# Kernel optimization log

Measured on AMD Instinct MI355X. Metric: run time of the kernel, lower is better.

## Reference

```python
import jax, jax.numpy as jnp
import numpy as np

N_Q_HEADS = 16
N_KV_HEADS = 4
HEAD_DIM = 128
SLIDING_WINDOW = 1024
ROPE_BASE = 1024


def _rope_tables(L, dim):
    # half-truncate RoPE: first dim//4 freqs geometric, next dim//4 zero
    freqs = (1.0 / ROPE_BASE) ** jnp.linspace(0.0, 1.0, num=dim // 4)
    freqs = jnp.concatenate([freqs, jnp.zeros(dim // 4, dtype=freqs.dtype)])
    theta = jnp.arange(L, dtype=jnp.float32)[:, None] * freqs[None, :]  # (L, dim/2)
    cos = jnp.cos(theta)[None, :, None, :]  # (1, L, 1, dim/2)
    sin = jnp.sin(theta)[None, :, None, :]
    return cos, sin


def _rotate(x, cos, sin):
    # x: (B, L, H, D)
    x1, x2 = jnp.split(x, 2, axis=-1)
    return jnp.concatenate([x1 * cos + x2 * sin, -x1 * sin + x2 * cos], axis=-1)


def setup_inputs() -> dict:
    key = jax.random.key(0)
    k1, k2, k3, k4 = jax.random.split(key, 4)
    B, L, D = 1, 2048, 2048
    qkv_dim = (N_Q_HEADS + 2 * N_KV_HEADS) * HEAD_DIM  # 3072
    return {
        "x": jax.random.normal(k1, (B, L, D), dtype=jnp.float32),
        "Wqkv": jax.random.normal(k2, (D, qkv_dim), dtype=jnp.float32) * (D ** -0.5),
        "Wo": jax.random.normal(k3, (N_Q_HEADS * HEAD_DIM, D), dtype=jnp.float32) * ((N_Q_HEADS * HEAD_DIM) ** -0.5),
        "s": jax.random.normal(k4, (1, N_Q_HEADS), dtype=jnp.float32) * 0.1,
    }


def reference(x, Wqkv, Wo, s):
    B, L, D = x.shape
    H, QM, hd = N_KV_HEADS, N_Q_HEADS // N_KV_HEADS, HEAD_DIM

    proj = x @ Wqkv  # (B, L, (Hq + 2*Hkv) * hd)
    q, k, v = jnp.split(proj, (N_Q_HEADS * hd, (N_Q_HEADS + N_KV_HEADS) * hd), axis=-1)

    cos, sin = _rope_tables(L, hd)
    q = _rotate(q.reshape(B, L, -1, hd), cos, sin).reshape(B, L, H, QM, hd)
    k = _rotate(k.reshape(B, L, H, hd), cos, sin)
    v = v.reshape(B, L, H, hd)

    sm_scale = 1.0 / jnp.sqrt(jnp.float32(hd))
    q_pos = jnp.arange(L)[None, :, None]
    k_pos = jnp.arange(L)[None, None, :]
    causal = q_pos >= k_pos                       # (1, L, L)
    window = q_pos < k_pos + SLIDING_WINDOW       # index % 2 == 0 -> window active
    mask = causal & window

    # (B, H, M, Lq, Lk) attention logits
    attn = jnp.einsum("bqhmd,bkhd->bhmqk", q, k) * sm_scale
    # NOTE: faithful to source: -inf placed WHERE mask is True
    attn = jnp.where(mask, -jnp.inf, attn)

    sink = jnp.broadcast_to(s.reshape(B, H, QM, 1, 1), (B, H, QM, L, 1))
    w = jax.nn.softmax(jnp.concatenate([attn, sink], axis=-1), axis=-1)[..., :-1]

    out = jnp.einsum("bhmqk,bkhd->bqhmd", w, v).reshape(B, L, -1)
    return out @ Wo
```

## Files before the change

kernel.cpp:

```cpp
#include <hip/hip_runtime.h>
#include <hip/hip_bf16.h>
#include <math.h>

typedef __bf16 bf16;
typedef __bf16 bf16x8 __attribute__((ext_vector_type(8)));
typedef __bf16 bf16x4v __attribute__((ext_vector_type(4)));
typedef short s16x4 __attribute__((ext_vector_type(4)));
typedef float f32x4 __attribute__((ext_vector_type(4)));

#define GLD16(gp, lp) __builtin_amdgcn_global_load_lds( \
    (__attribute__((address_space(1))) void*)(void*)(gp), \
    (__attribute__((address_space(3))) void*)(lp), 16, 0, 0)

#define L_SEQ 2048
#define D_MODEL 2048
#define QKV_N 3072
#define HD 128
#define QSCALE 0.1275310242959836f
#define LOG2E 1.4426950408889634f

__global__ __launch_bounds__(256) void prep(const float* __restrict__ x,
                                            const float* __restrict__ Wqkv,
                                            const float* __restrict__ Wo,
                                            bf16* __restrict__ xb,
                                            bf16* __restrict__ wqkvT,
                                            bf16* __restrict__ woT) {
    __shared__ float tile[32][33];
    int bid = blockIdx.x;
    if (bid < 4096) {
        int idx = (bid * 256 + threadIdx.x) * 4;
        float4 f = *(const float4*)(x + idx);
        bf16x4v o;
        o.x = (bf16)f.x; o.y = (bf16)f.y; o.z = (bf16)f.z; o.w = (bf16)f.w;
        *(bf16x4v*)(xb + idx) = o;
        return;
    }
    bid -= 4096;
    const float* src; bf16* dst; long ld_s, ld_d; int bx, by;
    if (bid < 6144) { bx = bid % 96; by = bid / 96; src = Wqkv; dst = wqkvT; ld_s = QKV_N; ld_d = D_MODEL; }
    else { bid -= 6144; bx = bid & 63; by = bid >> 6; src = Wo; dst = woT; ld_s = D_MODEL; ld_d = D_MODEL; }
    const int tx = threadIdx.x & 31, ty = threadIdx.x >> 5;
    const long c = bx * 32 + tx, r0 = by * 32;
#pragma unroll
    for (int i = 0; i < 4; ++i)
        tile[ty + i * 8][tx] = src[(r0 + ty + i * 8) * ld_s + c];
    __syncthreads();
    const long c0 = bx * 32;
#pragma unroll
    for (int i = 0; i < 4; ++i)
        dst[(c0 + ty + i * 8) * ld_d + r0 + tx] = (bf16)tile[tx][ty + i * 8];
}

__global__ __launch_bounds__(256, 3) void gemm_qkv(const bf16* __restrict__ A,
                                                   const bf16* __restrict__ Bt,
                                                   bf16* __restrict__ Qb,
                                                   bf16* __restrict__ Kb,
                                                   bf16* __restrict__ Vtb) {
    constexpr int KDIM = D_MODEL;
    __shared__ __align__(16) bf16 As[2][64 * 64];
    __shared__ __align__(16) bf16 Bs[2][128 * 64];
    const int tid = threadIdx.x;
    const int wid = tid >> 6, lane = tid & 63;
    const int quad = lane >> 4, l15 = lane & 15;
    const int wm = wid & 1, wn = wid >> 1;
    const int head = blockIdx.x;
    const long m0 = (long)blockIdx.y * 64, n0 = (long)head * 128;

    f32x4 acc[2][4];
#pragma unroll
    for (int i = 0; i < 2; ++i)
#pragma unroll
        for (int j = 0; j < 4; ++j) acc[i][j] = (f32x4){0.f, 0.f, 0.f, 0.f};

    const int srow8 = lane >> 3;
    const int schunk = lane & 7;

    auto stage = [&](int k0, int buf) {
#pragma unroll
        for (int ii = 0; ii < 2; ++ii) {
            const int rowb = wid * 16 + ii * 8;
            const int row = rowb + srow8;
            const int gcol = (schunk ^ (row & 7)) * 8;
            GLD16(A + (m0 + row) * KDIM + k0 + gcol, &As[buf][rowb * 64]);
        }
#pragma unroll
        for (int ii = 0; ii < 4; ++ii) {
            const int rowb = wid * 32 + ii * 8;
            const int row = rowb + srow8;
            const int gcol = (schunk ^ (row & 7)) * 8;
            GLD16(Bt + (n0 + row) * KDIM + k0 + gcol, &Bs[buf][rowb * 64]);
        }
    };
    stage(0, 0);

    for (int k0 = 0; k0 < KDIM; k0 += 64) {
        __syncthreads();
        if (k0 + 64 < KDIM) stage(k0 + 64, ((k0 >> 6) + 1) & 1);
        const int buf = (k0 >> 6) & 1;
#pragma unroll
        for (int ks = 0; ks < 2; ++ks) {
            const int pos = ((ks * 4 + quad) ^ (l15 & 7)) * 8;
            bf16x8 af[2], bfr[4];
#pragma unroll
            for (int i = 0; i < 2; ++i)
                af[i] = *(const bf16x8*)&As[buf][(wm * 32 + i * 16 + l15) * 64 + pos];
#pragma unroll
            for (int j = 0; j < 4; ++j)
                bfr[j] = *(const bf16x8*)&Bs[buf][(j * 32 + wn * 16 + l15) * 64 + pos];
#pragma unroll
            for (int i = 0; i < 2; ++i)
#pragma unroll
                for (int j = 0; j < 4; ++j)
                    acc[i][j] = __builtin_amdgcn_mfma_f32_16x16x32_bf16(af[i], bfr[j], acc[i][j], 0, 0, 0);
        }
    }

    if (head < 20) {
        const float sc = head < 16 ? QSCALE : 1.0f;
        bf16* dst = head < 16 ? Qb + (long)head * L_SEQ * HD
                              : Kb + (long)(head - 16) * L_SEQ * HD;
        const int d0 = wn * 16 + l15;
        const float freq = exp2f((float)d0 * (-10.0f / 31.0f));
        const int d1 = 32 + wn * 16 + l15;
#pragma unroll
        for (int i = 0; i < 2; ++i)
#pragma unroll
            for (int r = 0; r < 4; ++r) {
                const long row = m0 + wm * 32 + i * 16 + quad * 4 + r;
                float sn, cs;
                sincosf((float)row * freq, &sn, &cs);
                const float x1 = acc[i][0][r], x2 = acc[i][2][r];
                bf16* p = dst + row * HD;
                p[d0]      = (bf16)((x1 * cs + x2 * sn) * sc);
                p[d0 + 64] = (bf16)((x2 * cs - x1 * sn) * sc);
                p[d1]      = (bf16)(acc[i][1][r] * sc);
                p[d1 + 64] = (bf16)(acc[i][3][r] * sc);
            }
    } else {
        bf16* dst = Vtb + (long)(head - 20) * HD * L_SEQ;
#pragma unroll
        for (int i = 0; i < 2; ++i) {
            const long m = m0 + wm * 32 + i * 16 + quad * 4;
#pragma unroll
            for (int j = 0; j < 4; ++j) {
                const int d = j * 32 + wn * 16 + l15;
                bf16x4v vv;
#pragma unroll
                for (int r = 0; r < 4; ++r) vv[r] = (bf16)acc[i][j][r];
                *(bf16x4v*)(dst + (long)d * L_SEQ + m) = vv;
            }
        }
    }
}

__global__ __launch_bounds__(256, 4) void gemm_out(const bf16* __restrict__ A,
                                                   const bf16* __restrict__ Bt,
                                                   float* __restrict__ C) {
    constexpr int KDIM = D_MODEL;
    __shared__ __align__(16) bf16 As[2][64 * 64];
    __shared__ __align__(16) bf16 Bs[2][64 * 64];
    const int tid = threadIdx.x;
    const int wid = tid >> 6, lane = tid & 63;
    const int quad = lane >> 4, l15 = lane & 15;
    const int wm = wid & 1, wn = wid >> 1;
    const long m0 = (long)blockIdx.y * 64, n0 = (long)blockIdx.x * 64;

    f32x4 acc[2][2];
#pragma unroll
    for (int i = 0; i < 2; ++i)
#pragma unroll
        for (int j = 0; j < 2; ++j) acc[i][j] = (f32x4){0.f, 0.f, 0.f, 0.f};

    const int srow8 = lane >> 3;
    const int schunk = lane & 7;

    auto stage = [&](int k0, int buf) {
#pragma unroll
        for (int ii = 0; ii < 2; ++ii) {
            const int rowb = wid * 16 + ii * 8;
            const int row = rowb + srow8;
            const int gcol = (schunk ^ (row & 7)) * 8;
            GLD16(A + (m0 + row) * KDIM + k0 + gcol, &As[buf][rowb * 64]);
        }
#pragma unroll
        for (int ii = 0; ii < 2; ++ii) {
            const int rowb = wid * 16 + ii * 8;
            const int row = rowb + srow8;
            const int gcol = (schunk ^ (row & 7)) * 8;
            GLD16(Bt + (n0 + row) * KDIM + k0 + gcol, &Bs[buf][rowb * 64]);
        }
    };
    stage(0, 0);

    for (int k0 = 0; k0 < KDIM; k0 += 64) {
        __syncthreads();
        if (k0 + 64 < KDIM) stage(k0 + 64, ((k0 >> 6) + 1) & 1);
        const int buf = (k0 >> 6) & 1;
#pragma unroll
        for (int ks = 0; ks < 2; ++ks) {
            const int pos = ((ks * 4 + quad) ^ (l15 & 7)) * 8;
            bf16x8 af[2], bfr[2];
#pragma unroll
            for (int i = 0; i < 2; ++i)
                af[i] = *(const bf16x8*)&As[buf][(wm * 32 + i * 16 + l15) * 64 + pos];
#pragma unroll
            for (int j = 0; j < 2; ++j)
                bfr[j] = *(const bf16x8*)&Bs[buf][(wn * 32 + j * 16 + l15) * 64 + pos];
#pragma unroll
            for (int i = 0; i < 2; ++i)
#pragma unroll
                for (int j = 0; j < 2; ++j)
                    acc[i][j] = __builtin_amdgcn_mfma_f32_16x16x32_bf16(af[i], bfr[j], acc[i][j], 0, 0, 0);
        }
    }

#pragma unroll
    for (int i = 0; i < 2; ++i)
#pragma unroll
        for (int j = 0; j < 2; ++j) {
            const long row = m0 + wm * 32 + i * 16 + quad * 4;
            const long col = n0 + wn * 32 + j * 16 + l15;
#pragma unroll
            for (int r = 0; r < 4; ++r)
                C[(row + r) * (long)D_MODEL + col] = acc[i][j][r];
        }
}

__global__ __launch_bounds__(256, 2) void attn_p(const bf16* __restrict__ Qb,
                                                 const bf16* __restrict__ Kb,
                                                 const bf16* __restrict__ Vtb,
                                                 bf16* __restrict__ Opart,
                                                 float* __restrict__ lpart) {
    __shared__ __align__(1024) char smem[65536];

    const int bid = blockIdx.x;
    int t, hq, half;
    if (bid < 256) { t = bid >> 5; hq = (bid & 31) >> 1; half = bid & 1; }
    else { int b2 = bid - 256; t = 8 + (b2 >> 5); hq = (b2 & 31) >> 1; half = b2 & 1; }
    const int h = hq >> 2;
    const int q0 = t * 128;
    const int tid = threadIdx.x;
    const int w = tid >> 6;
    const int lane = tid & 63;
    const int quad = lane >> 4, l15 = lane & 15;

    const bf16* Qg = Qb + (long)hq * L_SEQ * HD;
    const bf16* Kg = Kb + (long)h * L_SEQ * HD;
    const bf16* Vg = Vtb + (long)h * HD * L_SEQ;

    bf16x8 qb[2][4];
#pragma unroll
    for (int rf = 0; rf < 2; ++rf)
#pragma unroll
        for (int kkd = 0; kkd < 4; ++kkd)
            qb[rf][kkd] = *(const bf16x8*)(Qg + (long)(q0 + w * 32 + rf * 16 + l15) * HD
                                              + kkd * 32 + quad * 8);

    f32x4 oaccT[2][8];
#pragma unroll
    for (int rf = 0; rf < 2; ++rf)
#pragma unroll
        for (int j = 0; j < 8; ++j) oaccT[rf][j] = (f32x4){0.f, 0.f, 0.f, 0.f};
    float lacc[2] = {0.f, 0.f};

    const int locnt = (2 * t - 14 > 0) ? (2 * t - 14) : 0;
    const int n = locnt + 32 - 2 * t;
    const int cnt = n >> 1;

    auto ktile = [&](int idx) {
        const int i = 2 * idx + half;
        return (i < locnt) ? i : (2 * t + (i - locnt));
    };

    auto stage = [&](int idx, int buf) {
        const int k0 = ktile(idx) * 64;
        bf16* Ksb  = (bf16*)(smem + buf * 32768);
        bf16* Vtsb = (bf16*)(smem + buf * 32768 + 16384);
#pragma unroll
        for (int ii = 0; ii < 4; ++ii) {
            int rowb = w * 16 + ii * 4;
            int row = rowb + quad;
            GLD16(Kg + (long)(k0 + row) * HD + ((l15 ^ (row & 7)) * 8), &Ksb[rowb * 128]);
        }
#pragma unroll
        for (int ii = 0; ii < 4; ++ii) {
            int rowb = w * 32 + ii * 8;
            int row = rowb + (lane >> 3);
            GLD16(Vg + (long)row * L_SEQ + k0 + (((lane & 7) ^ (row & 7)) * 8), &Vtsb[rowb * 64]);
        }
    };

    stage(0, 0);

    for (int it = 0; it < cnt; ++it) {
        __syncthreads();
        if (it + 1 < cnt) stage(it + 1, (it + 1) & 1);

        const int kt = ktile(it);
        const int k0 = kt * 64;
        const bf16* Ks  = (const bf16*)(smem + (it & 1) * 32768);
        const bf16* Vts = (const bf16*)(smem + (it & 1) * 32768 + 16384);

        f32x4 sacc[2][4];
#pragma unroll
        for (int kb = 0; kb < 4; ++kb) {
            bf16x8 ka[4];
#pragma unroll
            for (int kkd = 0; kkd < 4; ++kkd)
                ka[kkd] = *(const bf16x8*)&Ks[(kb * 16 + l15) * 128 +
                                              (((kkd * 4 + quad) ^ (l15 & 7)) * 8)];
#pragma unroll
            for (int rf = 0; rf < 2; ++rf) {
                f32x4 acc = (f32x4){0.f, 0.f, 0.f, 0.f};
#pragma unroll
                for (int kkd = 0; kkd < 4; ++kkd)
                    acc = __builtin_amdgcn_mfma_f32_16x16x32_bf16(ka[kkd], qb[rf][kkd], acc, 0, 0, 0);
                sacc[rf][kb] = acc;
            }
        }

        const bool bnd = (kt == 2 * t) || (kt == 2 * t + 1) ||
                         (kt == 2 * t - 15) || (kt == 2 * t - 16);
        s16x4 pb[2][4];
#pragma unroll
        for (int rf = 0; rf < 2; ++rf) {
            const int qq = q0 + w * 32 + rf * 16 + l15;
#pragma unroll
            for (int kb = 0; kb < 4; ++kb) {
#pragma unroll
                for (int r = 0; r < 4; ++r) {
                    float v = sacc[rf][kb][r];
                    if (bnd) {
                        const int kk = k0 + kb * 16 + quad * 4 + r;
                        if (!((kk > qq) || (kk <= qq - 1024))) v = -1e30f;
                    }
                    const float p = exp2f(v);
                    lacc[rf] += p;
                    bf16 hp = (bf16)p;
                    pb[rf][kb][r] = __builtin_bit_cast(short, hp);
                }
            }
        }

#pragma unroll
        for (int j = 0; j < 8; ++j) {
            const int drow = j * 16 + l15;
#pragma unroll
            for (int kq = 0; kq < 4; ++kq) {
                const int pc = ((kq * 2 + (quad >> 1)) ^ (l15 & 7));
                s16x4 va = *(const s16x4*)((const char*)&Vts[drow * 64] + pc * 16 + (quad & 1) * 8);
#pragma unroll
                for (int rf = 0; rf < 2; ++rf)
                    oaccT[rf][j] = __builtin_amdgcn_mfma_f32_16x16x16bf16_1k(
                        va, pb[rf][kq], oaccT[rf][j], 0, 0, 0);
            }
        }
    }

#pragma unroll
    for (int rf = 0; rf < 2; ++rf) {
        lacc[rf] += __shfl_xor(lacc[rf], 16, 64);
        lacc[rf] += __shfl_xor(lacc[rf], 32, 64);
    }

    bf16* Od = Opart + (long)bid * 16384;
#pragma unroll
    for (int rf = 0; rf < 2; ++rf) {
        const int ql = w * 32 + rf * 16 + l15;
#pragma unroll
        for (int j = 0; j < 8; ++j) {
            bf16x4v ov;
#pragma unroll
            for (int r = 0; r < 4; ++r) ov[r] = (bf16)oaccT[rf][j][r];
            *(bf16x4v*)(Od + ql * 128 + j * 16 + quad * 4) = ov;
        }
        if (quad == 0) lpart[bid * 128 + ql] = lacc[rf];
    }
}

__global__ __launch_bounds__(256) void attn_combine(const bf16* __restrict__ Opart,
                                                    const float* __restrict__ lpart,
                                                    const float* __restrict__ sink,
                                                    bf16* __restrict__ attnb) {
    const int job = blockIdx.x >> 3, sub = blockIdx.x & 7;
    const int t = job >> 4, hq = job & 15;
    const int bid0 = (t < 8) ? (t * 32 + hq * 2) : (256 + (t - 8) * 32 + hq * 2);
    const int bid1 = bid0 + 1;
    const int e = sub * 2048 + threadIdx.x * 8;
    const int q = e >> 7, d0 = e & 127;
    bf16x8 o0 = *(const bf16x8*)(Opart + (long)bid0 * 16384 + q * 128 + d0);
    bf16x8 o1 = *(const bf16x8*)(Opart + (long)bid1 * 16384 + q * 128 + d0);
    const float l = lpart[bid0 * 128 + q] + lpart[bid1 * 128 + q] +
                    exp2f(sink[hq] * LOG2E);
    const float inv = 1.0f / l;
    bf16x8 ov;
#pragma unroll
    for (int r = 0; r < 8; ++r)
        ov[r] = (bf16)(((float)o0[r] + (float)o1[r]) * inv);
    *(bf16x8*)(attnb + (long)(t * 128 + q) * D_MODEL + hq * 128 + d0) = ov;
}

extern "C" void kernel_launch(void* const* d_in, const int* in_sizes, int n_in,
                              void* d_out, int out_size, void* d_ws, size_t ws_size,
                              hipStream_t stream) {
    (void)in_sizes; (void)n_in; (void)out_size; (void)ws_size;
    const float* x    = (const float*)d_in[0];
    const float* Wqkv = (const float*)d_in[1];
    const float* Wo   = (const float*)d_in[2];
    const float* s    = (const float*)d_in[3];
    float* out = (float*)d_out;

    char* ws = (char*)d_ws;
    bf16* xb    = (bf16*)ws;
    bf16* wqkvT = (bf16*)(ws + 8388608);
    bf16* Qb    = (bf16*)(ws + 20971520);
    bf16* Kb    = (bf16*)(ws + 29360128);
    bf16* Vtb   = (bf16*)(ws + 31457280);
    bf16* woT   = (bf16*)(ws + 33554432);
    bf16* attnb = (bf16*)(ws + 41943040);
    bf16* Opart = (bf16*)ws;
    float* lpart = (float*)(ws + 16777216);

    prep<<<14336, 256, 0, stream>>>(x, Wqkv, Wo, xb, wqkvT, woT);

    gemm_qkv<<<dim3(QKV_N / 128, L_SEQ / 64), 256, 0, stream>>>(
        xb, wqkvT, Qb, Kb, Vtb);

    attn_p<<<512, 256, 0, stream>>>(Qb, Kb, Vtb, Opart, lpart);

    attn_combine<<<2048, 256, 0, stream>>>(Opart, lpart, s, attnb);

    gemm_out<<<dim3(D_MODEL / 64, L_SEQ / 64), 256, 0, stream>>>(
        attnb, woT, out);
}
```

Measured before the change: 215.0 us.

## Read K and V tiles directly from global memory instead of LDS staging

Removes the double-buffered LDS staging of K and V tiles and the per-iteration barrier in the attention kernel, loading MFMA operands straight from global memory through the cache. This is meant to cut LDS traffic and sync overhead and to free shared memory for higher occupancy. In exchange every wave fetches the same K/V data independently, with smaller, less coalesced loads and no explicit prefetch overlap, so the kernel relies on the L1/L2 caches to supply that reuse.

```diff
diff --git a/kernel.cpp b/kernel.cpp
--- a/kernel.cpp
+++ b/kernel.cpp
@@ -231,8 +231,6 @@
                                                  const bf16* __restrict__ Vtb,
                                                  bf16* __restrict__ Opart,
                                                  float* __restrict__ lpart) {
-    __shared__ __align__(1024) char smem[65536];
-
     const int bid = blockIdx.x;
     int t, hq, half;
     if (bid < 256) { t = bid >> 5; hq = (bid & 31) >> 1; half = bid & 1; }
@@ -272,34 +270,10 @@
         return (i < locnt) ? i : (2 * t + (i - locnt));
     };
 
-    auto stage = [&](int idx, int buf) {
-        const int k0 = ktile(idx) * 64;
-        bf16* Ksb  = (bf16*)(smem + buf * 32768);
-        bf16* Vtsb = (bf16*)(smem + buf * 32768 + 16384);
-#pragma unroll
-        for (int ii = 0; ii < 4; ++ii) {
-            int rowb = w * 16 + ii * 4;
-            int row = rowb + quad;
-            GLD16(Kg + (long)(k0 + row) * HD + ((l15 ^ (row & 7)) * 8), &Ksb[rowb * 128]);
-        }
-#pragma unroll
-        for (int ii = 0; ii < 4; ++ii) {
-            int rowb = w * 32 + ii * 8;
-            int row = rowb + (lane >> 3);
-            GLD16(Vg + (long)row * L_SEQ + k0 + (((lane & 7) ^ (row & 7)) * 8), &Vtsb[rowb * 64]);
-        }
-    };
-
-    stage(0, 0);
-
     for (int it = 0; it < cnt; ++it) {
-        __syncthreads();
-        if (it + 1 < cnt) stage(it + 1, (it + 1) & 1);
-
         const int kt = ktile(it);
         const int k0 = kt * 64;
-        const bf16* Ks  = (const bf16*)(smem + (it & 1) * 32768);
-        const bf16* Vts = (const bf16*)(smem + (it & 1) * 32768 + 16384);
+        const bf16* Kt = Kg + (long)k0 * HD;
 
         f32x4 sacc[2][4];
 #pragma unroll
@@ -307,8 +281,8 @@
             bf16x8 ka[4];
 #pragma unroll
             for (int kkd = 0; kkd < 4; ++kkd)
-                ka[kkd] = *(const bf16x8*)&Ks[(kb * 16 + l15) * 128 +
-                                              (((kkd * 4 + quad) ^ (l15 & 7)) * 8)];
+                ka[kkd] = *(const bf16x8*)(Kt + (long)(kb * 16 + l15) * HD
+                                              + kkd * 32 + quad * 8);
 #pragma unroll
             for (int rf = 0; rf < 2; ++rf) {
                 f32x4 acc = (f32x4){0.f, 0.f, 0.f, 0.f};
@@ -344,11 +318,10 @@
 
 #pragma unroll
         for (int j = 0; j < 8; ++j) {
-            const int drow = j * 16 + l15;
+            const bf16* Vrow = Vg + (long)(j * 16 + l15) * L_SEQ + k0;
 #pragma unroll
             for (int kq = 0; kq < 4; ++kq) {
-                const int pc = ((kq * 2 + (quad >> 1)) ^ (l15 & 7));
-                s16x4 va = *(const s16x4*)((const char*)&Vts[drow * 64] + pc * 16 + (quad & 1) * 8);
+                s16x4 va = *(const s16x4*)(Vrow + kq * 16 + quad * 4);
 #pragma unroll
                 for (int rf = 0; rf < 2; ++rf)
                     oaccT[rf][j] = __builtin_amdgcn_mfma_f32_16x16x16bf16_1k(
```

Result: slower. 313.7 us (+45.9%).

## Fuse split-attention combine into output-projection GEMM A-tile loading

Applied to the files above, without the earlier changes.

Removes the separate attn_combine kernel and its bf16 attention buffer. gemm_out now loads the two partial attention outputs and their softmax denominators (plus sink) into registers, normalizes them, and writes the bf16 A tile into LDS itself. The aim is to save one launch and the write-then-read round trip of the combined attention tensor. In exchange, each GEMM block reads twice as much A data, redoes the normalization for every N-tile column, and replaces async global-to-LDS loads for A with register-staged loads.

```diff
diff --git a/kernel.cpp b/kernel.cpp
--- a/kernel.cpp
+++ b/kernel.cpp
@@ -153,7 +153,9 @@
     }
 }
 
-__global__ __launch_bounds__(256, 4) void gemm_out(const bf16* __restrict__ A,
+__global__ __launch_bounds__(256, 4) void gemm_out(const bf16* __restrict__ Opart,
+                                                   const float* __restrict__ lpart,
+                                                   const float* __restrict__ sink,
                                                    const bf16* __restrict__ Bt,
                                                    float* __restrict__ C) {
     constexpr int KDIM = D_MODEL;
@@ -165,6 +167,10 @@
     const int wm = wid & 1, wn = wid >> 1;
     const long m0 = (long)blockIdx.y * 64, n0 = (long)blockIdx.x * 64;
 
+    const int t = (int)(m0 >> 7);
+    const int qlb = (int)(m0 & 64);
+    const int bidbase = (t < 8) ? t * 32 : 256 + (t - 8) * 32;
+
     f32x4 acc[2][2];
 #pragma unroll
     for (int i = 0; i < 2; ++i)
@@ -174,14 +180,40 @@
     const int srow8 = lane >> 3;
     const int schunk = lane & 7;
 
-    auto stage = [&](int k0, int buf) {
+    bf16x8 o0ST[2], o1ST[2];
+    float l0ST[2], l1ST[2], skST;
+
+    auto aload = [&](int k0) {
+        const int hq = k0 >> 7;
+        const int dbase = k0 & 64;
+        const int bid0 = bidbase + hq * 2;
+        skST = sink[hq];
 #pragma unroll
         for (int ii = 0; ii < 2; ++ii) {
-            const int rowb = wid * 16 + ii * 8;
-            const int row = rowb + srow8;
+            const int row = wid * 16 + ii * 8 + srow8;
             const int gcol = (schunk ^ (row & 7)) * 8;
-            GLD16(A + (m0 + row) * KDIM + k0 + gcol, &As[buf][rowb * 64]);
-        }
+            const int ql = qlb + row;
+            const bf16* p0 = Opart + (long)bid0 * 16384 + ql * 128 + dbase + gcol;
+            o0ST[ii] = *(const bf16x8*)p0;
+            o1ST[ii] = *(const bf16x8*)(p0 + 16384);
+            l0ST[ii] = lpart[bid0 * 128 + ql];
+            l1ST[ii] = lpart[bid0 * 128 + 128 + ql];
+        }
+    };
+    auto awrite = [&](int buf) {
+        const float sk = exp2f(skST * LOG2E);
+#pragma unroll
+        for (int ii = 0; ii < 2; ++ii) {
+            const int row = wid * 16 + ii * 8 + srow8;
+            const float inv = 1.0f / (l0ST[ii] + l1ST[ii] + sk);
+            bf16x8 av;
+#pragma unroll
+            for (int r = 0; r < 8; ++r)
+                av[r] = (bf16)(((float)o0ST[ii][r] + (float)o1ST[ii][r]) * inv);
+            *(bf16x8*)&As[buf][row * 64 + schunk * 8] = av;
+        }
+    };
+    auto bstage = [&](int k0, int buf) {
 #pragma unroll
         for (int ii = 0; ii < 2; ++ii) {
             const int rowb = wid * 16 + ii * 8;
@@ -190,12 +222,14 @@
             GLD16(Bt + (n0 + row) * KDIM + k0 + gcol, &Bs[buf][rowb * 64]);
         }
     };
-    stage(0, 0);
+
+    aload(0); bstage(0, 0); awrite(0);
 
     for (int k0 = 0; k0 < KDIM; k0 += 64) {
         __syncthreads();
-        if (k0 + 64 < KDIM) stage(k0 + 64, ((k0 >> 6) + 1) & 1);
         const int buf = (k0 >> 6) & 1;
+        const bool more = (k0 + 64 < KDIM);
+        if (more) { aload(k0 + 64); bstage(k0 + 64, buf ^ 1); }
 #pragma unroll
         for (int ks = 0; ks < 2; ++ks) {
             const int pos = ((ks * 4 + quad) ^ (l15 & 7)) * 8;
@@ -212,6 +246,7 @@
                 for (int j = 0; j < 2; ++j)
                     acc[i][j] = __builtin_amdgcn_mfma_f32_16x16x32_bf16(af[i], bfr[j], acc[i][j], 0, 0, 0);
         }
+        if (more) awrite(buf ^ 1);
     }
 
 #pragma unroll
@@ -378,28 +413,6 @@
     }
 }
 
-__global__ __launch_bounds__(256) void attn_combine(const bf16* __restrict__ Opart,
-                                                    const float* __restrict__ lpart,
-                                                    const float* __restrict__ sink,
-                                                    bf16* __restrict__ attnb) {
-    const int job = blockIdx.x >> 3, sub = blockIdx.x & 7;
-    const int t = job >> 4, hq = job & 15;
-    const int bid0 = (t < 8) ? (t * 32 + hq * 2) : (256 + (t - 8) * 32 + hq * 2);
-    const int bid1 = bid0 + 1;
-    const int e = sub * 2048 + threadIdx.x * 8;
-    const int q = e >> 7, d0 = e & 127;
-    bf16x8 o0 = *(const bf16x8*)(Opart + (long)bid0 * 16384 + q * 128 + d0);
-    bf16x8 o1 = *(const bf16x8*)(Opart + (long)bid1 * 16384 + q * 128 + d0);
-    const float l = lpart[bid0 * 128 + q] + lpart[bid1 * 128 + q] +
-                    exp2f(sink[hq] * LOG2E);
-    const float inv = 1.0f / l;
-    bf16x8 ov;
-#pragma unroll
-    for (int r = 0; r < 8; ++r)
-        ov[r] = (bf16)(((float)o0[r] + (float)o1[r]) * inv);
-    *(bf16x8*)(attnb + (long)(t * 128 + q) * D_MODEL + hq * 128 + d0) = ov;
-}
-
 extern "C" void kernel_launch(void* const* d_in, const int* in_sizes, int n_in,
                               void* d_out, int out_size, void* d_ws, size_t ws_size,
                               hipStream_t stream) {
@@ -417,7 +430,6 @@
     bf16* Kb    = (bf16*)(ws + 29360128);
     bf16* Vtb   = (bf16*)(ws + 31457280);
     bf16* woT   = (bf16*)(ws + 33554432);
-    bf16* attnb = (bf16*)(ws + 41943040);
     bf16* Opart = (bf16*)ws;
     float* lpart = (float*)(ws + 16777216);
 
@@ -428,8 +440,6 @@
 
     attn_p<<<512, 256, 0, stream>>>(Qb, Kb, Vtb, Opart, lpart);
 
-    attn_combine<<<2048, 256, 0, stream>>>(Opart, lpart, s, attnb);
-
     gemm_out<<<dim3(D_MODEL / 64, L_SEQ / 64), 256, 0, stream>>>(
-        attnb, woT, out);
+        Opart, lpart, s, woT, out);
 }
```

Result: slower. 228.5 us (+6.2%).
